# Performance work log

Hardware: AMD Instinct MI355X
Metric: run time of the kernel (lower is better)

Reference implementation:

```python
import jax, jax.numpy as jnp
import numpy as np

B, N, D, H, DFF, V, L, ASTHOP = 16, 512, 256, 8, 1024, 50000, 2, 2
NEG_INF = -1e9
LRELU_SLOPE = 0.2
LN_EPS = 1e-6


def positional_encoding(length, d):
    pos = np.arange(length)[:, None].astype(np.float32)
    i = np.arange(d)[None, :].astype(np.float32)
    angle = pos / np.power(10000.0, (2.0 * np.floor(i / 2.0)) / d)
    pe = np.zeros((length, d), dtype=np.float32)
    pe[:, 0::2] = np.sin(angle[:, 0::2])
    pe[:, 1::2] = np.cos(angle[:, 1::2])
    return jnp.asarray(pe[None])  # [1, length, d]


def layer_norm(x, g, b):
    mu = jnp.mean(x, axis=-1, keepdims=True)
    var = jnp.mean((x - mu) ** 2, axis=-1, keepdims=True)
    return (x - mu) * jax.lax.rsqrt(var + LN_EPS) * g + b


def setup_inputs() -> dict:
    key = jax.random.key(0)
    ks = jax.random.split(key, 16)
    s = 0.02
    f32 = jnp.float32
    return {
        "node_input": jax.random.randint(ks[0], (B, N), 0, V, dtype=jnp.int32),
        "edge_input": jax.random.randint(ks[1], (B, N, N), 0, 2, dtype=jnp.int32),
        "mha_mask": jnp.zeros((B, 1, 1, N), jnp.int32),
        "training": 0,
        "embed": jax.random.normal(ks[2], (V, D), f32) * s,
        "Wg": jax.random.normal(ks[3], (D, D), f32) * s,
        "a1": jax.random.normal(ks[4], (D, 1), f32) * s,
        "a2": jax.random.normal(ks[5], (D, 1), f32) * s,
        "Wq": jax.random.normal(ks[6], (L, D, D), f32) * s,
        "bq": jnp.zeros((L, D), f32),
        "Wk": jax.random.normal(ks[7], (L, D, D), f32) * s,
        "bk": jnp.zeros((L, D), f32),
        "Wv": jax.random.normal(ks[8], (L, D, D), f32) * s,
        "bv": jnp.zeros((L, D), f32),
        "Wo": jax.random.normal(ks[9], (L, D, D), f32) * s,
        "bo": jnp.zeros((L, D), f32),
        "W1": jax.random.normal(ks[10], (L, D, DFF), f32) * s,
        "b1": jnp.zeros((L, DFF), f32),
        "W2": jax.random.normal(ks[11], (L, DFF, D), f32) * s,
        "b2": jnp.zeros((L, D), f32),
        "ln1_g": jnp.ones((L, D), f32),
        "ln1_b": jnp.zeros((L, D), f32),
        "ln2_g": jnp.ones((L, D), f32),
        "ln2_b": jnp.zeros((L, D), f32),
    }


def reference(node_input, edge_input, mha_mask, training, embed, Wg, a1, a2,
              Wq, bq, Wk, bk, Wv, bv, Wo, bo, W1, b1, W2, b2,
              ln1_g, ln1_b, ln2_g, ln2_b):
    del training  # inference: dropout is identity
    pe = positional_encoding(N, D)
    adj = edge_input > 0  # [B,N,N] bool

    x = embed[node_input]  # [B,N,D] embedding lookup
    # --- GAT message-passing hops (shared weights) ---
    for _ in range(ASTHOP):
        h = x @ Wg  # [B,N,D]
        # e_ij = LeakyReLU(a1.h_i + a2.h_j)
        e = jax.nn.leaky_relu(h @ a1 + jnp.swapaxes(h @ a2, 1, 2), LRELU_SLOPE)
        e = jnp.where(adj, e, NEG_INF)
        alpha = jax.nn.softmax(e, axis=-1)  # [B,N,N]
        x = jax.nn.elu(jnp.einsum('bij,bjd->bid', alpha, h))

    # --- scale + positional encoding ---
    x = x * jnp.sqrt(jnp.float32(D)) + pe[:, :N, :]

    # --- transformer encoder stack ---
    mask = mha_mask.astype(x.dtype)  # [B,1,1,N], 1 = pad
    dh = D // H
    attn = None
    for l in range(L):
        q = (x @ Wq[l] + bq[l]).reshape(B, N, H, dh).transpose(0, 2, 1, 3)
        k = (x @ Wk[l] + bk[l]).reshape(B, N, H, dh).transpose(0, 2, 1, 3)
        v = (x @ Wv[l] + bv[l]).reshape(B, N, H, dh).transpose(0, 2, 1, 3)
        scores = jnp.einsum('bhqd,bhkd->bhqk', q, k) / jnp.sqrt(jnp.float32(dh))
        scores = scores + mask * NEG_INF
        attn = jax.nn.softmax(scores, axis=-1)  # [B,H,N,N]
        o = jnp.einsum('bhqk,bhkd->bhqd', attn, v).transpose(0, 2, 1, 3).reshape(B, N, D)
        x = layer_norm(x + o @ Wo[l] + bo[l], ln1_g[l], ln1_b[l])
        f = jax.nn.relu(x @ W1[l] + b1[l]) @ W2[l] + b2[l]
        x = layer_norm(x + f, ln2_g[l], ln2_b[l])
    return (x, attn)
```

## Files before the change

### kernel.cpp

```cpp
#include <hip/hip_runtime.h>
#include <math.h>

#define B_    16
#define N_    512
#define D_    256
#define H_    8
#define DH_   32
#define DFF_  1024
#define L_    2
#define NEG_INF_ (-1e9f)
#define LRELU_ 0.2f

typedef __attribute__((ext_vector_type(8))) short bf8_t;
typedef __attribute__((ext_vector_type(8))) unsigned short us8;
typedef __attribute__((ext_vector_type(4))) float f4_t;

__device__ __forceinline__ unsigned short f2bf(float f) {
    union { float f; unsigned u; } v; v.f = f;
    unsigned r = v.u + 0x7FFF + ((v.u >> 16) & 1);
    return (unsigned short)(r >> 16);
}
__device__ __forceinline__ float bf2f(unsigned short h) {
    union { unsigned u; float f; } v; v.u = ((unsigned)h) << 16;
    return v.f;
}

__device__ __forceinline__ void gl_lds16(const void* g, void* l) {
    __builtin_amdgcn_global_load_lds(
        (const __attribute__((address_space(1))) unsigned int*)g,
        (__attribute__((address_space(3))) unsigned int*)l, 16, 0, 0);
}

template <int BM, int BN, int WROWS, int WCOLS>
__global__ __launch_bounds__(256) void mfma_gemm(
    const unsigned short* __restrict__ Ag, const unsigned short* __restrict__ Btg,
    const float* __restrict__ bias,
    float* __restrict__ Cfg, unsigned short* __restrict__ Chg, int trans,
    int K, int lda, int ldb, int ldc,
    int inner, long sAo, long sAi, long sBo, long sBi, long sCo, long sCi,
    float scale, int act)
{
    constexpr int TM = BM / WROWS, TN = BN / WCOLS;
    constexpr int MT = TM / 16, NT = TN / 16;

    int z  = blockIdx.z;
    int zo = z / inner;
    int zi = z - zo * inner;
    const unsigned short* Ab = Ag + (long)zo * sAo + (long)zi * sAi;
    const unsigned short* Bt = Btg + (long)zo * sBo + (long)zi * sBi;
    long co = (long)zo * sCo + (long)zi * sCi;

    int bm = blockIdx.y * BM;
    int bn = blockIdx.x * BN;
    int tid  = threadIdx.x;
    int lane = tid & 63;
    int w    = tid >> 6;
    int wr   = w / WCOLS, wc = w - wr * WCOLS;

    __shared__ unsigned short As[2][BM * 32];
    __shared__ unsigned short Bs[2][BN * 32];

    f4_t acc[MT][NT] = {};

    int lrow = lane & 15;
    int koff = (lane >> 4) * 8;

    auto stage = [&](int buf, int k0) {
#pragma unroll
        for (int t = w; t < BM / 16; t += 4) {
            int s = t * 512 + lane * 8;
            int r = s >> 5, c = s & 31;
            gl_lds16(Ab + (long)(bm + r) * lda + k0 + c, &As[buf][t * 512]);
        }
#pragma unroll
        for (int t = w; t < BN / 16; t += 4) {
            int s = t * 512 + lane * 8;
            int r = s >> 5, c = s & 31;
            gl_lds16(Bt + (long)(bn + r) * ldb + k0 + c, &Bs[buf][t * 512]);
        }
    };

    int nk = K >> 5;
    stage(0, 0);
    __syncthreads();

    for (int t = 0; t < nk; t++) {
        int cur = t & 1;
        if (t + 1 < nk) stage(cur ^ 1, (t + 1) << 5);

        bf8_t af[MT], bfr[NT];
#pragma unroll
        for (int mi = 0; mi < MT; mi++)
            af[mi] = *(const bf8_t*)&As[cur][(wr * TM + mi * 16 + lrow) * 32 + koff];
#pragma unroll
        for (int ni = 0; ni < NT; ni++)
            bfr[ni] = *(const bf8_t*)&Bs[cur][(wc * TN + ni * 16 + lrow) * 32 + koff];
#pragma unroll
        for (int mi = 0; mi < MT; mi++)
#pragma unroll
            for (int ni = 0; ni < NT; ni++)
                acc[mi][ni] = __builtin_amdgcn_mfma_f32_16x16x32_bf16(
                    af[mi], bfr[ni], acc[mi][ni], 0, 0, 0);
        __syncthreads();
    }

#pragma unroll
    for (int mi = 0; mi < MT; mi++) {
#pragma unroll
        for (int ni = 0; ni < NT; ni++) {
            int row0 = bm + wr * TM + mi * 16 + (lane >> 4) * 4;
            int col  = bn + wc * TN + ni * 16 + (lane & 15);
            float bv = bias ? bias[col] : 0.f;
            float vv[4];
#pragma unroll
            for (int r = 0; r < 4; r++) {
                float v = acc[mi][ni][r] * scale + bv;
                if (act == 1) v = fmaxf(v, 0.f);
                else if (act == 2) v = v > 0.f ? v : (__expf(v) - 1.f);
                vv[r] = v;
            }
            if (trans) {
                ushort4 u = make_ushort4(f2bf(vv[0]), f2bf(vv[1]), f2bf(vv[2]), f2bf(vv[3]));
                *(ushort4*)&Chg[co + (long)col * ldc + row0] = u;
            } else {
                if (Cfg) {
#pragma unroll
                    for (int r = 0; r < 4; r++)
                        Cfg[co + (long)(row0 + r) * ldc + col] = vv[r];
                }
                if (Chg) {
#pragma unroll
                    for (int r = 0; r < 4; r++)
                        Chg[co + (long)(row0 + r) * ldc + col] = f2bf(vv[r]);
                }
            }
        }
    }
}

template <bool WRITE_ATTN>
__global__ __launch_bounds__(256) void attn_fused(
    const unsigned short* __restrict__ QKV,
    const int* __restrict__ mask,
    float* __restrict__ attn_out,
    unsigned short* __restrict__ Ob)
{
    int bh = blockIdx.x;
    int b  = bh >> 3, h = bh & 7;
    int q0 = blockIdx.y * 64;
    int tid  = threadIdx.x;
    int lane = tid & 63, w = tid >> 6;
    int lrow = lane & 15, quad = lane >> 4;

    __shared__ unsigned short Ks[512 * 40];
    __shared__ unsigned short Vs[32 * 136];
    __shared__ float maskf[512];
    unsigned short* Ps = Ks;

    const long tokbase = (long)b * N_;

#pragma unroll
    for (int i = 0; i < 8; i++) {
        int idx = tid + i * 256;
        int row = idx >> 2, seg = idx & 3;
        us8 v = *(const us8*)&QKV[(tokbase + row) * 768 + 256 + h * 32 + seg * 8];
        *(us8*)&Ks[row * 40 + seg * 8] = v;
    }
    maskf[tid]       = (float)mask[b * N_ + tid] * NEG_INF_;
    maskf[tid + 256] = (float)mask[b * N_ + tid + 256] * NEG_INF_;

    bf8_t aq = *(const bf8_t*)&QKV[(tokbase + q0 + w * 16 + lrow) * 768 + h * 32 + quad * 8];
    __syncthreads();

    f4_t acc[32];
    f4_t zero = {0.f, 0.f, 0.f, 0.f};
#pragma unroll
    for (int ni = 0; ni < 32; ni++) {
        bf8_t bk = *(const bf8_t*)&Ks[(ni * 16 + lrow) * 40 + quad * 8];
        acc[ni] = __builtin_amdgcn_mfma_f32_16x16x32_bf16(aq, bk, zero, 0, 0, 0);
    }

    const float rscale = 0.17677669529663687f;
    float mr[4] = {-3e38f, -3e38f, -3e38f, -3e38f};
#pragma unroll
    for (int ni = 0; ni < 32; ni++) {
        float mk = maskf[ni * 16 + lrow];
#pragma unroll
        for (int r = 0; r < 4; r++) {
            float v = acc[ni][r] * rscale + mk;
            acc[ni][r] = v;
            mr[r] = fmaxf(mr[r], v);
        }
    }
#pragma unroll
    for (int r = 0; r < 4; r++) {
        mr[r] = fmaxf(mr[r], __shfl_xor(mr[r], 1));
        mr[r] = fmaxf(mr[r], __shfl_xor(mr[r], 2));
        mr[r] = fmaxf(mr[r], __shfl_xor(mr[r], 4));
        mr[r] = fmaxf(mr[r], __shfl_xor(mr[r], 8));
    }
    float sr[4] = {0.f, 0.f, 0.f, 0.f};
#pragma unroll
    for (int ni = 0; ni < 32; ni++) {
#pragma unroll
        for (int r = 0; r < 4; r++) {
            float p = __expf(acc[ni][r] - mr[r]);
            acc[ni][r] = p;
            sr[r] += p;
        }
    }
#pragma unroll
    for (int r = 0; r < 4; r++) {
        sr[r] += __shfl_xor(sr[r], 1);
        sr[r] += __shfl_xor(sr[r], 2);
        sr[r] += __shfl_xor(sr[r], 4);
        sr[r] += __shfl_xor(sr[r], 8);
        sr[r] = 1.f / sr[r];
    }
#pragma unroll
    for (int ni = 0; ni < 32; ni++)
#pragma unroll
        for (int r = 0; r < 4; r++)
            acc[ni][r] *= sr[r];

    if (WRITE_ATTN) {
#pragma unroll
        for (int ni = 0; ni < 32; ni++) {
#pragma unroll
            for (int r = 0; r < 4; r++)
                attn_out[((long)bh * N_ + q0 + w * 16 + quad * 4 + r) * N_ + ni * 16 + lrow]
                    = acc[ni][r];
        }
    }

    f4_t oacc[2] = {{0.f,0.f,0.f,0.f}, {0.f,0.f,0.f,0.f}};
    for (int c = 0; c < 4; c++) {
        __syncthreads();
        {
            int kk = tid >> 1, dseg = (tid & 1) * 16;
            const unsigned short* src =
                &QKV[(tokbase + c * 128 + kk) * 768 + 512 + h * 32 + dseg];
            us8 v0 = *(const us8*)src;
            us8 v1 = *(const us8*)(src + 8);
#pragma unroll
            for (int jj = 0; jj < 8; jj++) {
                Vs[(dseg + jj) * 136 + kk]     = v0[jj];
                Vs[(dseg + 8 + jj) * 136 + kk] = v1[jj];
            }
        }
#pragma unroll
        for (int ni = 0; ni < 8; ni++) {
            int nn = c * 8 + ni;
#pragma unroll
            for (int r = 0; r < 4; r++)
                Ps[w * 2176 + (quad * 4 + r) * 136 + ni * 16 + lrow] = f2bf(acc[nn][r]);
        }
        __syncthreads();
#pragma unroll
        for (int k8 = 0; k8 < 4; k8++) {
            bf8_t ap = *(const bf8_t*)&Ps[w * 2176 + lrow * 136 + k8 * 32 + quad * 8];
#pragma unroll
            for (int t = 0; t < 2; t++) {
                bf8_t bvf = *(const bf8_t*)&Vs[(t * 16 + lrow) * 136 + k8 * 32 + quad * 8];
                oacc[t] = __builtin_amdgcn_mfma_f32_16x16x32_bf16(ap, bvf, oacc[t], 0, 0, 0);
            }
        }
    }

#pragma unroll
    for (int t = 0; t < 2; t++)
#pragma unroll
        for (int r = 0; r < 4; r++)
            Ob[(tokbase + q0 + w * 16 + quad * 4 + r) * 256 + h * 32 + t * 16 + lrow]
                = f2bf(oacc[t][r]);
}

struct ConvJobs {
    const float* src[13];
    unsigned short* dst[13];
    int R[13];
    int C[13];
};

__global__ __launch_bounds__(256) void conv_transpose(ConvJobs j)
{
    int z = blockIdx.z;
    int R = j.R[z], C = j.C[z];
    int r0 = blockIdx.y * 64, c0 = blockIdx.x * 64;
    if (r0 >= R || c0 >= C) return;
    __shared__ float t[64][65];
    const float* src = j.src[z];
    unsigned short* dst = j.dst[z];
    int tx = threadIdx.x & 63, ty = threadIdx.x >> 6;
#pragma unroll
    for (int i = 0; i < 16; i++) {
        int r = ty + i * 4;
        t[r][tx] = src[(long)(r0 + r) * C + c0 + tx];
    }
    __syncthreads();
#pragma unroll
    for (int i = 0; i < 16; i++) {
        int c = ty + i * 4;
        dst[(long)(c0 + c) * R + r0 + tx] = f2bf(t[tx][c]);
    }
}

__global__ __launch_bounds__(256) void pack_bias(const float* __restrict__ bq,
                                                 const float* __restrict__ bk,
                                                 const float* __restrict__ bv,
                                                 float* __restrict__ bc)
{
    int i = blockIdx.x * 256 + threadIdx.x;
    int l = i / 768, c = i - l * 768;
    float v = (c < 256) ? bq[l * 256 + c]
            : (c < 512) ? bk[l * 256 + c - 256]
                        : bv[l * 256 + c - 512];
    bc[i] = v;
}

__global__ __launch_bounds__(64) void gather_embed(const int* __restrict__ idx,
                                                   const float* __restrict__ embed,
                                                   float* __restrict__ X,
                                                   unsigned short* __restrict__ Xb)
{
    int row = blockIdx.x;
    int id  = idx[row];
    float4 v = ((const float4*)(embed + (long)id * D_))[threadIdx.x];
    ((float4*)(X + (long)row * D_))[threadIdx.x] = v;
    ((ushort4*)(Xb + (long)row * D_))[threadIdx.x] =
        make_ushort4(f2bf(v.x), f2bf(v.y), f2bf(v.z), f2bf(v.w));
}

__global__ __launch_bounds__(256) void gat_s12T(const unsigned short* __restrict__ hT,
                                                const float* __restrict__ a1,
                                                const float* __restrict__ a2,
                                                float* __restrict__ s1,
                                                float* __restrict__ s2)
{
    int lane = threadIdx.x & 63;
    int dq   = threadIdx.x >> 6;
    int j = blockIdx.x * 64 + lane;
    float d1 = 0.f, d2 = 0.f;
#pragma unroll 8
    for (int d = dq * 64; d < dq * 64 + 64; d++) {
        float hv = bf2f(hT[(long)d * (B_ * N_) + j]);
        d1 += hv * a1[d];
        d2 += hv * a2[d];
    }
    __shared__ float r1[4][64], r2[4][64];
    r1[dq][lane] = d1;
    r2[dq][lane] = d2;
    __syncthreads();
    if (dq == 0) {
        s1[j] = r1[0][lane] + r1[1][lane] + r1[2][lane] + r1[3][lane];
        s2[j] = r2[0][lane] + r2[1][lane] + r2[2][lane] + r2[3][lane];
    }
}

__global__ __launch_bounds__(256) void gat_alpha(const float* __restrict__ s1,
                                                 const float* __restrict__ s2,
                                                 const int* __restrict__ edges,
                                                 unsigned short* __restrict__ alpha)
{
    int row = blockIdx.x;
    int b   = row >> 9;
    const int*   erow = edges + (long)row * N_;
    const float* s2b  = s2 + (long)b * N_;
    float si = s1[row];
    int t = threadIdx.x;

    float e  = si + s2b[t];
    e = e > 0.f ? e : LRELU_ * e;
    float v0 = (erow[t] > 0) ? e : NEG_INF_;
    float e2 = si + s2b[t + 256];
    e2 = e2 > 0.f ? e2 : LRELU_ * e2;
    float v1 = (erow[t + 256] > 0) ? e2 : NEG_INF_;

    __shared__ float redm[4], reds[4];
    float m = fmaxf(v0, v1);
    for (int off = 32; off; off >>= 1) m = fmaxf(m, __shfl_xor(m, off));
    if ((t & 63) == 0) redm[t >> 6] = m;
    __syncthreads();
    m = fmaxf(fmaxf(redm[0], redm[1]), fmaxf(redm[2], redm[3]));
    float x0 = __expf(v0 - m), x1 = __expf(v1 - m);
    float s = x0 + x1;
    for (int off = 32; off; off >>= 1) s += __shfl_xor(s, off);
    if ((t & 63) == 0) reds[t >> 6] = s;
    __syncthreads();
    s = reds[0] + reds[1] + reds[2] + reds[3];
    float inv = 1.f / s;
    alpha[(long)row * N_ + t]       = f2bf(x0 * inv);
    alpha[(long)row * N_ + t + 256] = f2bf(x1 * inv);
}

__global__ __launch_bounds__(64) void ln_add(const float* __restrict__ x,
                                             const float* __restrict__ tm,
                                             const float* __restrict__ g,
                                             const float* __restrict__ bta,
                                             float* __restrict__ out,
                                             unsigned short* __restrict__ outb)
{
    long row  = blockIdx.x;
    int  lane = threadIdx.x;
    float4 xv = ((const float4*)(x + row * D_))[lane];
    float4 tv = ((const float4*)(tm + row * D_))[lane];
    float4 v = make_float4(xv.x + tv.x, xv.y + tv.y, xv.z + tv.z, xv.w + tv.w);
    float s = v.x + v.y + v.z + v.w;
    for (int off = 32; off; off >>= 1) s += __shfl_xor(s, off);
    float mean = s * (1.f / D_);
    float4 d = make_float4(v.x - mean, v.y - mean, v.z - mean, v.w - mean);
    float sq = d.x * d.x + d.y * d.y + d.z * d.z + d.w * d.w;
    for (int off = 32; off; off >>= 1) sq += __shfl_xor(sq, off);
    float rs = rsqrtf(sq * (1.f / D_) + 1e-6f);
    float4 gv = ((const float4*)g)[lane];
    float4 bv = ((const float4*)bta)[lane];
    float4 o = make_float4(d.x * rs * gv.x + bv.x, d.y * rs * gv.y + bv.y,
                           d.z * rs * gv.z + bv.z, d.w * rs * gv.w + bv.w);
    ((float4*)(out + row * D_))[lane] = o;
    if (outb)
        ((ushort4*)(outb + row * D_))[lane] =
            make_ushort4(f2bf(o.x), f2bf(o.y), f2bf(o.z), f2bf(o.w));
}

__global__ __launch_bounds__(256) void scale_pe(float* __restrict__ X,
                                                unsigned short* __restrict__ Xb)
{
    int row = blockIdx.x;
    int n = row & (N_ - 1);
    int d = threadIdx.x;
    float expo = (float)(d & ~1) * (1.0f / D_);
    float inv  = __expf(-expo * 9.210340371976184f);
    float ang  = (float)n * inv;
    float pe   = (d & 1) ? cosf(ang) : sinf(ang);
    long idx = (long)row * D_ + d;
    float v = X[idx] * 16.0f + pe;
    X[idx]  = v;
    Xb[idx] = f2bf(v);
}

extern "C" void kernel_launch(void* const* d_in, const int* in_sizes, int n_in,
                              void* d_out, int out_size, void* d_ws, size_t ws_size,
                              hipStream_t stream)
{
    const int*   node  = (const int*)d_in[0];
    const int*   edge  = (const int*)d_in[1];
    const int*   mask  = (const int*)d_in[2];
    const float* embed = (const float*)d_in[4];
    const float* Wg    = (const float*)d_in[5];
    const float* a1    = (const float*)d_in[6];
    const float* a2    = (const float*)d_in[7];
    const float* Wq    = (const float*)d_in[8];
    const float* bq    = (const float*)d_in[9];
    const float* Wk    = (const float*)d_in[10];
    const float* bk    = (const float*)d_in[11];
    const float* Wv    = (const float*)d_in[12];
    const float* bv    = (const float*)d_in[13];
    const float* Wo    = (const float*)d_in[14];
    const float* bo    = (const float*)d_in[15];
    const float* W1    = (const float*)d_in[16];
    const float* b1    = (const float*)d_in[17];
    const float* W2    = (const float*)d_in[18];
    const float* b2    = (const float*)d_in[19];
    const float* ln1g  = (const float*)d_in[20];
    const float* ln1b  = (const float*)d_in[21];
    const float* ln2g  = (const float*)d_in[22];
    const float* ln2b  = (const float*)d_in[23];

    const long XSZ = (long)B_ * N_ * D_;
    const int  MR  = B_ * N_;
    float* outx = (float*)d_out;
    float* ATT  = outx + XSZ;

    float*          X    = (float*)d_ws;
    unsigned short* Xb   = (unsigned short*)(X + XSZ);
    float*          Hb   = (float*)(Xb + XSZ);
    unsigned short* alphab = (unsigned short*)Hb;
    unsigned short* QKVb = (unsigned short*)(Hb + XSZ);
    unsigned short* hT   = QKVb;
    unsigned short* Ob   = QKVb + (long)MR * 768;
    unsigned short* Fb   = Ob + XSZ;
    float* S1 = (float*)(Fb + (long)MR * DFF_);
    float* S2 = S1 + MR;
    unsigned short* WgT = (unsigned short*)(S2 + MR);
    unsigned short* Wc  = WgT + 65536;
    unsigned short* WoT = Wc + 2 * 768 * 256;
    unsigned short* W1T = WoT + 2 * 65536;
    unsigned short* W2T = W1T + 2 * 262144;
    float*          bc  = (float*)(W2T + 2 * 262144);

    ConvJobs j;
    j.src[0] = Wg;  j.dst[0] = WgT;  j.R[0] = 256;  j.C[0] = 256;
    for (int l = 0; l < 2; l++) {
        j.src[1 + l] = Wq + l * 65536;  j.dst[1 + l] = Wc + l * 196608;           j.R[1+l] = 256;  j.C[1+l] = 256;
        j.src[3 + l] = Wk + l * 65536;  j.dst[3 + l] = Wc + l * 196608 + 65536;   j.R[3+l] = 256;  j.C[3+l] = 256;
        j.src[5 + l] = Wv + l * 65536;  j.dst[5 + l] = Wc + l * 196608 + 131072;  j.R[5+l] = 256;  j.C[5+l] = 256;
        j.src[7 + l] = Wo + l * 65536;  j.dst[7 + l] = WoT + l * 65536;           j.R[7+l] = 256;  j.C[7+l] = 256;
        j.src[9 + l] = W1 + l * 262144; j.dst[9 + l] = W1T + l * 262144;          j.R[9+l] = 256;  j.C[9+l] = 1024;
        j.src[11+ l] = W2 + l * 262144; j.dst[11+ l] = W2T + l * 262144;          j.R[11+l]= 1024; j.C[11+l]= 256;
    }
    conv_transpose<<<dim3(16, 16, 13), 256, 0, stream>>>(j);
    pack_bias<<<6, 256, 0, stream>>>(bq, bk, bv, bc);

    gather_embed<<<MR, 64, 0, stream>>>(node, embed, X, Xb);

    for (int hop = 0; hop < 2; hop++) {
        mfma_gemm<64,128,1,4><<<dim3(2, 128, 1), 256, 0, stream>>>(
            Xb, WgT, nullptr, nullptr, hT, 1,
            256, 256, 256, MR, 1, 0,0, 0,0, 0,0, 1.f, 0);
        gat_s12T<<<128, 256, 0, stream>>>(hT, a1, a2, S1, S2);
        gat_alpha<<<MR, 256, 0, stream>>>(S1, S2, edge, alphab);
        mfma_gemm<64,128,1,4><<<dim3(2, 8, 16), 256, 0, stream>>>(
            alphab, hT, nullptr, X, Xb, 0,
            512, 512, MR, 256, 1,
            (long)N_*N_, 0, (long)N_, 0, (long)N_*D_, 0, 1.f, 2);
    }

    scale_pe<<<MR, 256, 0, stream>>>(X, Xb);

    for (int l = 0; l < L_; l++) {
        mfma_gemm<64,128,1,4><<<dim3(6, 128, 1), 256, 0, stream>>>(
            Xb, Wc + l * 196608, bc + l * 768, nullptr, QKVb, 0,
            256, 256, 256, 768, 1, 0,0, 0,0, 0,0, 1.f, 0);

        if (l == L_ - 1)
            attn_fused<true><<<dim3(128, 8, 1), 256, 0, stream>>>(QKVb, mask, ATT, Ob);
        else
            attn_fused<false><<<dim3(128, 8, 1), 256, 0, stream>>>(QKVb, mask, nullptr, Ob);

        mfma_gemm<64,128,1,4><<<dim3(2, 128, 1), 256, 0, stream>>>(
            Ob, WoT + l * 65536, bo + l * D_, Hb, nullptr, 0,
            256, 256, 256, 256, 1, 0,0, 0,0, 0,0, 1.f, 0);
        ln_add<<<MR, 64, 0, stream>>>(X, Hb, ln1g + l * D_, ln1b + l * D_, X, Xb);

        mfma_gemm<128,128,2,2><<<dim3(8, 64, 1), 256, 0, stream>>>(
            Xb, W1T + l * 262144, b1 + l * DFF_, nullptr, Fb, 0,
            256, 256, 256, 1024, 1, 0,0, 0,0, 0,0, 1.f, 1);
        mfma_gemm<64,128,1,4><<<dim3(2, 128, 1), 256, 0, stream>>>(
            Fb, W2T + l * 262144, b2 + l * D_, Hb, nullptr, 0,
            1024, 1024, 1024, 256, 1, 0,0, 0,0, 0,0, 1.f, 0);
        if (l == L_ - 1)
            ln_add<<<MR, 64, 0, stream>>>(X, Hb, ln2g + l * D_, ln2b + l * D_, outx, nullptr);
        else
            ln_add<<<MR, 64, 0, stream>>>(X, Hb, ln2g + l * D_, ln2b + l * D_, X, Xb);
    }
}
```

Before: 539.9 us.

## Fuse output-projection and FFN2 GEMMs with residual add and LayerNorm

Adds a GEMM kernel with a full 256-wide output row per block (32 rows x 256 cols) so bias, residual add and LayerNorm can be done in the epilogue with cross-wave reductions through shared memory. This replaces the Wo and W2 GEMMs plus the separate ln_add kernels, removing the fp32 intermediate round trip and four launches per layer. It also reworks the V-tile transpose into LDS to use 4x4 register transposes with vectorized stores. The risk is a smaller grid (256 blocks) and lower per-block parallelism for the K=1024 GEMM. In-place residual read/write of X is safe because each block owns its rows.

Result: no change. 536.7 us (-0.6%).

```diff
diff --git a/kernel.cpp b/kernel.cpp
--- a/kernel.cpp
+++ b/kernel.cpp
@@ -13,6 +13,7 @@
 
 typedef __attribute__((ext_vector_type(8))) short bf8_t;
 typedef __attribute__((ext_vector_type(8))) unsigned short us8;
+typedef __attribute__((ext_vector_type(4))) unsigned short us4;
 typedef __attribute__((ext_vector_type(4))) float f4_t;
 
 __device__ __forceinline__ unsigned short f2bf(float f) {
@@ -138,6 +139,158 @@
     }
 }
 
+__global__ __launch_bounds__(256) void mfma_gemm_ln(
+    const unsigned short* __restrict__ Ag, const unsigned short* __restrict__ Btg,
+    const float* __restrict__ bias,
+    const float* __restrict__ resid,
+    const float* __restrict__ g, const float* __restrict__ beta,
+    float* __restrict__ outf, unsigned short* __restrict__ outb,
+    int K)
+{
+    int bm = blockIdx.x * 32;
+    int tid = threadIdx.x, lane = tid & 63, w = tid >> 6;
+    int lrow = lane & 15, quad = lane >> 4;
+    int koff = quad * 8;
+
+    __shared__ unsigned short As[2][32 * 32];
+    __shared__ unsigned short Bs[2][256 * 32];
+    __shared__ float rsum[4][32];
+    __shared__ float rsq[4][32];
+
+    f4_t acc[2][4] = {};
+
+    auto stage = [&](int buf, int k0) {
+        if (w < 2) {
+            int s = w * 512 + lane * 8;
+            int r = s >> 5, c = s & 31;
+            gl_lds16(Ag + (long)(bm + r) * K + k0 + c, &As[buf][w * 512]);
+        }
+#pragma unroll
+        for (int t = w; t < 16; t += 4) {
+            int s = t * 512 + lane * 8;
+            int r = s >> 5, c = s & 31;
+            gl_lds16(Btg + (long)r * K + k0 + c, &Bs[buf][t * 512]);
+        }
+    };
+
+    int nk = K >> 5;
+    stage(0, 0);
+    __syncthreads();
+    for (int t = 0; t < nk; t++) {
+        int cur = t & 1;
+        if (t + 1 < nk) stage(cur ^ 1, (t + 1) << 5);
+        bf8_t af[2], bfr[4];
+#pragma unroll
+        for (int mi = 0; mi < 2; mi++)
+            af[mi] = *(const bf8_t*)&As[cur][(mi * 16 + lrow) * 32 + koff];
+#pragma unroll
+        for (int ni = 0; ni < 4; ni++)
+            bfr[ni] = *(const bf8_t*)&Bs[cur][(w * 64 + ni * 16 + lrow) * 32 + koff];
+#pragma unroll
+        for (int mi = 0; mi < 2; mi++)
+#pragma unroll
+            for (int ni = 0; ni < 4; ni++)
+                acc[mi][ni] = __builtin_amdgcn_mfma_f32_16x16x32_bf16(
+                    af[mi], bfr[ni], acc[mi][ni], 0, 0, 0);
+        __syncthreads();
+    }
+
+    float vv[2][4][4];
+    float sp[2][4] = {};
+#pragma unroll
+    for (int mi = 0; mi < 2; mi++)
+#pragma unroll
+        for (int ni = 0; ni < 4; ni++) {
+            int row = mi * 16 + quad * 4;
+            int col = w * 64 + ni * 16 + lrow;
+            float bcol = bias[col];
+#pragma unroll
+            for (int r = 0; r < 4; r++) {
+                float v = acc[mi][ni][r] + bcol +
+                          resid[(long)(bm + row + r) * 256 + col];
+                vv[mi][ni][r] = v;
+                sp[mi][r] += v;
+            }
+        }
+#pragma unroll
+    for (int mi = 0; mi < 2; mi++)
+#pragma unroll
+        for (int r = 0; r < 4; r++) {
+            float s = sp[mi][r];
+            s += __shfl_xor(s, 1); s += __shfl_xor(s, 2);
+            s += __shfl_xor(s, 4); s += __shfl_xor(s, 8);
+            sp[mi][r] = s;
+        }
+    if (lrow == 0) {
+#pragma unroll
+        for (int mi = 0; mi < 2; mi++)
+#pragma unroll
+            for (int r = 0; r < 4; r++)
+                rsum[w][mi * 16 + quad * 4 + r] = sp[mi][r];
+    }
+    __syncthreads();
+    float mean[2][4];
+#pragma unroll
+    for (int mi = 0; mi < 2; mi++)
+#pragma unroll
+        for (int r = 0; r < 4; r++) {
+            int row = mi * 16 + quad * 4 + r;
+            mean[mi][r] = (rsum[0][row] + rsum[1][row] + rsum[2][row] + rsum[3][row])
+                          * (1.f / 256.f);
+        }
+    float qp[2][4] = {};
+#pragma unroll
+    for (int mi = 0; mi < 2; mi++)
+#pragma unroll
+        for (int ni = 0; ni < 4; ni++)
+#pragma unroll
+            for (int r = 0; r < 4; r++) {
+                float d = vv[mi][ni][r] - mean[mi][r];
+                qp[mi][r] += d * d;
+            }
+#pragma unroll
+    for (int mi = 0; mi < 2; mi++)
+#pragma unroll
+        for (int r = 0; r < 4; r++) {
+            float s = qp[mi][r];
+            s += __shfl_xor(s, 1); s += __shfl_xor(s, 2);
+            s += __shfl_xor(s, 4); s += __shfl_xor(s, 8);
+            qp[mi][r] = s;
+        }
+    if (lrow == 0) {
+#pragma unroll
+        for (int mi = 0; mi < 2; mi++)
+#pragma unroll
+            for (int r = 0; r < 4; r++)
+                rsq[w][mi * 16 + quad * 4 + r] = qp[mi][r];
+    }
+    __syncthreads();
+    float rstd[2][4];
+#pragma unroll
+    for (int mi = 0; mi < 2; mi++)
+#pragma unroll
+        for (int r = 0; r < 4; r++) {
+            int row = mi * 16 + quad * 4 + r;
+            float var = (rsq[0][row] + rsq[1][row] + rsq[2][row] + rsq[3][row])
+                        * (1.f / 256.f);
+            rstd[mi][r] = rsqrtf(var + 1e-6f);
+        }
+#pragma unroll
+    for (int mi = 0; mi < 2; mi++)
+#pragma unroll
+        for (int ni = 0; ni < 4; ni++) {
+            int col = w * 64 + ni * 16 + lrow;
+            float gc = g[col], bc2 = beta[col];
+#pragma unroll
+            for (int r = 0; r < 4; r++) {
+                long orow = bm + mi * 16 + quad * 4 + r;
+                float o = (vv[mi][ni][r] - mean[mi][r]) * rstd[mi][r] * gc + bc2;
+                outf[orow * 256 + col] = o;
+                if (outb) outb[orow * 256 + col] = f2bf(o);
+            }
+        }
+}
+
 template <bool WRITE_ATTN>
 __global__ __launch_bounds__(256) void attn_fused(
     const unsigned short* __restrict__ QKV,
@@ -234,18 +387,20 @@
     }
 
     f4_t oacc[2] = {{0.f,0.f,0.f,0.f}, {0.f,0.f,0.f,0.f}};
+    int kk4 = (tid & 31) * 4;
+    int d0  = (tid >> 5) * 4;
     for (int c = 0; c < 4; c++) {
         __syncthreads();
         {
-            int kk = tid >> 1, dseg = (tid & 1) * 16;
-            const unsigned short* src =
-                &QKV[(tokbase + c * 128 + kk) * 768 + 512 + h * 32 + dseg];
-            us8 v0 = *(const us8*)src;
-            us8 v1 = *(const us8*)(src + 8);
-#pragma unroll
-            for (int jj = 0; jj < 8; jj++) {
-                Vs[(dseg + jj) * 136 + kk]     = v0[jj];
-                Vs[(dseg + 8 + jj) * 136 + kk] = v1[jj];
+            us4 vr[4];
+#pragma unroll
+            for (int i = 0; i < 4; i++)
+                vr[i] = *(const us4*)&QKV[(tokbase + c * 128 + kk4 + i) * 768
+                                          + 512 + h * 32 + d0];
+#pragma unroll
+            for (int jj = 0; jj < 4; jj++) {
+                us4 wv = { vr[0][jj], vr[1][jj], vr[2][jj], vr[3][jj] };
+                *(us4*)&Vs[(d0 + jj) * 136 + kk4] = wv;
             }
         }
 #pragma unroll
@@ -391,35 +546,6 @@
     float inv = 1.f / s;
     alpha[(long)row * N_ + t]       = f2bf(x0 * inv);
     alpha[(long)row * N_ + t + 256] = f2bf(x1 * inv);
-}
-
-__global__ __launch_bounds__(64) void ln_add(const float* __restrict__ x,
-                                             const float* __restrict__ tm,
-                                             const float* __restrict__ g,
-                                             const float* __restrict__ bta,
-                                             float* __restrict__ out,
-                                             unsigned short* __restrict__ outb)
-{
-    long row  = blockIdx.x;
-    int  lane = threadIdx.x;
-    float4 xv = ((const float4*)(x + row * D_))[lane];
-    float4 tv = ((const float4*)(tm + row * D_))[lane];
-    float4 v = make_float4(xv.x + tv.x, xv.y + tv.y, xv.z + tv.z, xv.w + tv.w);
-    float s = v.x + v.y + v.z + v.w;
-    for (int off = 32; off; off >>= 1) s += __shfl_xor(s, off);
-    float mean = s * (1.f / D_);
-    float4 d = make_float4(v.x - mean, v.y - mean, v.z - mean, v.w - mean);
-    float sq = d.x * d.x + d.y * d.y + d.z * d.z + d.w * d.w;
-    for (int off = 32; off; off >>= 1) sq += __shfl_xor(sq, off);
-    float rs = rsqrtf(sq * (1.f / D_) + 1e-6f);
-    float4 gv = ((const float4*)g)[lane];
-    float4 bv = ((const float4*)bta)[lane];
-    float4 o = make_float4(d.x * rs * gv.x + bv.x, d.y * rs * gv.y + bv.y,
-                           d.z * rs * gv.z + bv.z, d.w * rs * gv.w + bv.w);
-    ((float4*)(out + row * D_))[lane] = o;
-    if (outb)
-        ((ushort4*)(outb + row * D_))[lane] =
-            make_ushort4(f2bf(o.x), f2bf(o.y), f2bf(o.z), f2bf(o.w));
 }
 
 __global__ __launch_bounds__(256) void scale_pe(float* __restrict__ X,
@@ -527,20 +653,20 @@
         else
             attn_fused<false><<<dim3(128, 8, 1), 256, 0, stream>>>(QKVb, mask, nullptr, Ob);
 
-        mfma_gemm<64,128,1,4><<<dim3(2, 128, 1), 256, 0, stream>>>(
-            Ob, WoT + l * 65536, bo + l * D_, Hb, nullptr, 0,
-            256, 256, 256, 256, 1, 0,0, 0,0, 0,0, 1.f, 0);
-        ln_add<<<MR, 64, 0, stream>>>(X, Hb, ln1g + l * D_, ln1b + l * D_, X, Xb);
+        mfma_gemm_ln<<<dim3(MR / 32), 256, 0, stream>>>(
+            Ob, WoT + l * 65536, bo + l * D_, X,
+            ln1g + l * D_, ln1b + l * D_, X, Xb, 256);
 
         mfma_gemm<128,128,2,2><<<dim3(8, 64, 1), 256, 0, stream>>>(
             Xb, W1T + l * 262144, b1 + l * DFF_, nullptr, Fb, 0,
             256, 256, 256, 1024, 1, 0,0, 0,0, 0,0, 1.f, 1);
-        mfma_gemm<64,128,1,4><<<dim3(2, 128, 1), 256, 0, stream>>>(
-            Fb, W2T + l * 262144, b2 + l * D_, Hb, nullptr, 0,
-            1024, 1024, 1024, 256, 1, 0,0, 0,0, 0,0, 1.f, 0);
         if (l == L_ - 1)
-            ln_add<<<MR, 64, 0, stream>>>(X, Hb, ln2g + l * D_, ln2b + l * D_, outx, nullptr);
+            mfma_gemm_ln<<<dim3(MR / 32), 256, 0, stream>>>(
+                Fb, W2T + l * 262144, b2 + l * D_, X,
+                ln2g + l * D_, ln2b + l * D_, outx, nullptr, 1024);
         else
-            ln_add<<<MR, 64, 0, stream>>>(X, Hb, ln2g + l * D_, ln2b + l * D_, X, Xb);
-    }
-}
+            mfma_gemm_ln<<<dim3(MR / 32), 256, 0, stream>>>(
+                Fb, W2T + l * 262144, b2 + l * D_, X,
+                ln2g + l * D_, ln2b + l * D_, X, Xb, 1024);
+    }
+}
```
